# Performance work log

Hardware: AMD Instinct MI355X
Metric: run time of the kernel (lower is better)

The kernel has to match this reference:

```python
import jax, jax.numpy as jnp
import numpy as np

BETA = 0.01
EPS = 1e-6

def conv3x3(x, w, b):
    y = jax.lax.conv_general_dilated(x, w, (1, 1), 'SAME',
                                     dimension_numbers=('NCHW', 'OIHW', 'NCHW'))
    return y + b[None, :, None, None]

def variance_depth_flow(gt, patch, max_depth):
    B, C, H, W = gt.shape
    py, px = H // patch, W // patch
    # [B,C,py,px,P,P]
    p = gt.reshape(B, C, py, patch, px, patch).transpose(0, 1, 2, 4, 3, 5)
    p = jnp.where((p > 0.1) & (p < max_depth), p, jnp.zeros_like(p))
    bn = jnp.log(p[..., 0, :] + EPS)   # north border  [B,C,py,px,P]
    bs = jnp.log(p[..., -1, :] + EPS)  # south
    bw = jnp.log(p[..., :, 0] + EPS)   # west
    be = jnp.log(p[..., :, -1] + EPS)  # east
    def sx(b):  # shift patches left along x (axis=3), zero-pad last column
        return jnp.concatenate([b[:, :, :, 1:], jnp.zeros_like(b[:, :, :, :1])], axis=3)
    def sy(b):  # shift patches up along y (axis=2), zero-pad last row
        return jnp.concatenate([b[:, :, 1:], jnp.zeros_like(b[:, :, :1])], axis=2)
    diffs = [be - sx(bw), bs - sy(bn), be - sx(be), bs - sy(bs), bw - sx(bw),
             bn - sy(bn), bs - sx(bs), be - sy(be), bn - sx(bn), bw - sy(bw)]
    d = jnp.stack([x.sum(-1) for x in diffs], axis=-1)  # [B,C,py,px,10]
    d = d[:, 0].transpose(0, 3, 1, 2) / patch            # [B,10,py,px]
    return d

def smooth_l1(pred, target, beta):
    d = pred - target
    ad = jnp.abs(d)
    return jnp.where(ad < beta, 0.5 * d * d / beta, ad - 0.5 * beta)

def setup_inputs() -> dict:
    key = jax.random.key(0)
    ks = jax.random.split(key, 7)
    B, FC, DC, hw, HW = 32, 256, 64, 64, 512
    feat = jax.random.normal(ks[0], (B, FC, hw, hw), dtype=jnp.float32)
    depth = jax.random.normal(ks[1], (B, DC, hw, hw), dtype=jnp.float32)
    gts = jax.random.uniform(ks[2], (B, 1, HW, HW), dtype=jnp.float32)
    W_att = jax.random.normal(ks[3], (DC, FC, 3, 3), dtype=jnp.float32) * 0.02
    b_att = jnp.zeros((DC,), dtype=jnp.float32)
    W_post = jax.random.normal(ks[4], (10, DC, 3, 3), dtype=jnp.float32) * 0.05
    b_post = jnp.zeros((10,), dtype=jnp.float32)
    return {"feat": feat, "depth": depth, "gts": gts,
            "W_att": W_att, "b_att": b_att, "W_post": W_post, "b_post": b_post}

def reference(feat, depth, gts, W_att, b_att, W_post, b_post):
    max_depth = 80.0
    n, c, h, w = depth.shape
    patch = gts.shape[2] // h
    flow_gradient = variance_depth_flow(gts, patch, max_depth)  # [B,10,h,w]
    att = jax.nn.sigmoid(conv3x3(feat, W_att, b_att))           # [B,DC,h,w]
    ds = conv3x3(att * depth, W_post, b_post)                   # [B,10,h,w]
    diff = smooth_l1(ds, flow_gradient, BETA)
    return diff.sum() / (h * w * ds.shape[0] * ds.shape[1])
```

## Files before the change

kernel.cpp:

```cpp
#include <hip/hip_runtime.h>
#include <hip/hip_bf16.h>


typedef __attribute__((ext_vector_type(4))) float f32x4;
typedef __attribute__((ext_vector_type(8))) short s16x8;

#define DEVFN __device__ __forceinline__

DEVFN float bf2f(unsigned short u){
  unsigned int x = ((unsigned int)u) << 16;
  float f; __builtin_memcpy(&f, &x, 4); return f;
}
DEVFN unsigned short f2bf(float f){
  unsigned int x; __builtin_memcpy(&x, &f, 4);
  x += 0x7fffu + ((x >> 16) & 1u);
  return (unsigned short)(x >> 16);
}

#define ASYNC16(gp, lp) __builtin_amdgcn_global_load_lds( \
    (const __attribute__((address_space(1))) unsigned int*)(gp), \
    (__attribute__((address_space(3))) unsigned int*)(lp), 16, 0, 0)

__global__ void k_weights(const float* __restrict__ Watt, const float* __restrict__ Wpost,
                          unsigned short* __restrict__ WT1, unsigned short* __restrict__ WT2){
  const int t = blockIdx.x * 256 + threadIdx.x;
  const int n1 = 9 * 64 * 256;
  if (t < n1){
    const int tap = t / (64 * 256);
    const int rem = t % (64 * 256);
    const int oc = rem / 256, ic = rem % 256;
    WT1[t] = f2bf(Watt[(oc * 256 + ic) * 9 + tap]);
  }
  const int n2 = 9 * 16 * 64;
  if (t < n2){
    const int tap = t / (16 * 64);
    const int rem = t % (16 * 64);
    const int od = rem / 64, ic = rem % 64;
    const float v = (od < 10) ? Wpost[(od * 64 + ic) * 9 + tap] : 0.0f;
    WT2[t] = f2bf(v);
  }
}

__global__ void k_borders(const float* __restrict__ gts, float* __restrict__ S,
                          float* __restrict__ out){
  const int bid = blockIdx.x, tid = threadIdx.x;
  if (bid == 0 && tid == 0) *out = 0.0f;
  __shared__ float slab[4096];
  const int rel = bid;
  const float* gp = gts + (size_t)rel * 4096;
#pragma unroll
  for (int it = 0; it < 4; ++it){
    const int id = it * 256 + tid;
    *(f32x4*)&slab[id * 4] = *(const f32x4*)&gp[id * 4];
  }
  __syncthreads();
  const int px = tid & 63, border = tid >> 6;
  float s = 0.0f;
#pragma unroll
  for (int i = 0; i < 8; ++i){
    float v;
    if (border == 0)      v = slab[px * 8 + i];
    else if (border == 1) v = slab[7 * 512 + px * 8 + i];
    else if (border == 2) v = slab[i * 512 + px * 8];
    else                  v = slab[i * 512 + px * 8 + 7];
    v = ((v > 0.1f) && (v < 80.0f)) ? v : 0.0f;
    s += __logf(v + 1e-6f);
  }
  S[((size_t)rel * 64 + px) * 4 + border] = s;
}

__global__ __launch_bounds__(256, 2) void k_gemm1(
    const float* __restrict__ feat,
    const unsigned short* __restrict__ WT1,
    const float* __restrict__ batt,
    const float* __restrict__ depth,
    unsigned short* __restrict__ adT)
{
  __shared__ unsigned short As[6 * 66 * 32];
  __shared__ unsigned short Bs[576 * 32];
  const int t = threadIdx.x;
  const int l = t & 63, w = t >> 6;
  const int b = blockIdx.x >> 4, ytile = blockIdx.x & 15;
  const int y0 = ytile * 4;
  const int fr = l & 15, g = l >> 4;
  const int x = l;

  f32x4 acc[4][4];
#pragma unroll
  for (int i = 0; i < 4; ++i)
#pragma unroll
    for (int j = 0; j < 4; ++j)
#pragma unroll
      for (int q = 0; q < 4; ++q) acc[i][j][q] = 0.0f;

  if (t < 48){
    const int yy = t >> 3, k = t & 7;
    const int xp = (k & 1) ? 65 : 0;
    s16x8 z = {0,0,0,0,0,0,0,0};
    *(s16x8*)&As[(yy * 66 + xp) * 32 + (k >> 1) * 8] = z;
  }

  const int xp = x + 1;
  const int sx = (xp >> 1) & 3;
  const int slotB = (g ^ ((fr >> 1) & 3)) * 8;

  for (int c = 0; c < 8; ++c){
    float rr[48];
#pragma unroll
    for (int j = 0; j < 6; ++j){
      const int yr = y0 - 1 + j;
      if (yr >= 0 && yr < 64){
        const float* gp = feat + ((size_t)(b * 256 + c * 32 + w * 8)) * 4096
                               + (size_t)yr * 64 + x;
#pragma unroll
        for (int e = 0; e < 8; ++e) rr[j * 8 + e] = gp[(size_t)e * 4096];
      } else {
#pragma unroll
        for (int e = 0; e < 8; ++e) rr[j * 8 + e] = 0.0f;
      }
    }
#pragma unroll
    for (int it = 0; it < 9; ++it){
      const int idx = it * 256 + t;
      const int row = idx >> 2;
      const int sg = (idx & 3) ^ ((row >> 1) & 3);
      ASYNC16(WT1 + (size_t)row * 256 + c * 32 + sg * 8, &Bs[(size_t)idx * 8]);
    }
#pragma unroll
    for (int j = 0; j < 6; ++j){
      s16x8 v;
#pragma unroll
      for (int e = 0; e < 8; ++e) v[e] = (short)f2bf(rr[j * 8 + e]);
      *(s16x8*)&As[(j * 66 + xp) * 32 + ((w ^ sx) * 8)] = v;
    }
    __syncthreads();

    for (int tap = 0; tap < 9; ++tap){
      const int dy = tap / 3 - 1, dxp = tap % 3;
      const int r = fr + dxp;
      const int slotA = (g ^ ((r >> 1) & 3)) * 8;
      const int rowb = ((w + dy + 1) * 66 + r) * 32 + slotA;
      s16x8 af[4], bfr[4];
#pragma unroll
      for (int i = 0; i < 4; ++i) af[i] = *(const s16x8*)&As[rowb + i * 512];
#pragma unroll
      for (int j = 0; j < 4; ++j)
        bfr[j] = *(const s16x8*)&Bs[(tap * 64 + j * 16 + fr) * 32 + slotB];
#pragma unroll
      for (int i = 0; i < 4; ++i)
#pragma unroll
        for (int j = 0; j < 4; ++j)
          acc[i][j] = __builtin_amdgcn_mfma_f32_16x16x32_bf16(af[i], bfr[j], acc[i][j], 0, 0, 0);
    }
    __syncthreads();
  }

  const int y = y0 + w;
#pragma unroll
  for (int j = 0; j < 4; ++j){
    const int oc = j * 16 + fr;
    const float bb = batt[oc];
    const float* dpt = depth + ((size_t)(b * 64 + oc)) * 4096 + (size_t)y * 64;
    unsigned short* op = adT + ((size_t)(b * 4096 + y * 64)) * 64 + oc;
#pragma unroll
    for (int i = 0; i < 4; ++i){
#pragma unroll
      for (int q = 0; q < 4; ++q){
        const int xo = i * 16 + g * 4 + q;
        const float v = acc[i][j][q] + bb;
        const float att = 1.0f / (1.0f + __expf(-v));
        op[(size_t)xo * 64] = f2bf(att * dpt[xo]);
      }
    }
  }
}

DEVFN float sel4(f32x4 v, int i){
  const float ab = (i & 1) ? v[1] : v[0];
  const float cd = (i & 1) ? v[3] : v[2];
  return (i & 2) ? cd : ab;
}

__global__ __launch_bounds__(512, 2) void k_gemm2(
    const unsigned short* __restrict__ adT,
    const unsigned short* __restrict__ WT2,
    const float* __restrict__ bpost,
    const f32x4* __restrict__ S,
    float* __restrict__ out)
{
  __shared__ unsigned short As[2][20480];
  __shared__ unsigned short Bs[9216];
  __shared__ float ps[8];
  const int t = threadIdx.x;
  const int l = t & 63, w = t >> 6;
  const int b = blockIdx.x >> 3, ytile = blockIdx.x & 7;
  const int y0 = ytile * 8;
  const int fr = l & 15, g = l >> 4;

  f32x4 acc[4];
#pragma unroll
  for (int i = 0; i < 4; ++i)
#pragma unroll
    for (int q = 0; q < 4; ++q) acc[i][q] = 0.0f;

  auto stageA = [&](int c, int d){
#pragma unroll
    for (int it2 = 0; it2 < 5; ++it2){
      const int it = it2 * 2 + (t >> 8);
      const int yy = y0 - 1 + it;
      const int xx = (t >> 2) & 63, icg = t & 3;
      unsigned short* lp = &As[d][(it * 64 + xx) * 32 + icg * 8];
      if (yy >= 0 && yy < 64){
        const int sg = icg ^ ((xx >> 1) & 3);
        const unsigned short* gp = adT
            + ((size_t)(b * 4096 + yy * 64 + xx)) * 64 + c * 32 + sg * 8;
        ASYNC16(gp, lp);
      } else {
        s16x8 z = {0,0,0,0,0,0,0,0};
        *(s16x8*)lp = z;
      }
    }
  };
#pragma unroll
  for (int it = 0; it < 3; ++it){
    const int idx = it * 512 + t;
    if (idx < 1152){
      const int row = idx >> 3, p = idx & 7;
      const int sg = p ^ (row & 7);
      ASYNC16(WT2 + (size_t)row * 64 + sg * 8, Bs + (size_t)idx * 8);
    }
  }
  stageA(0, 0);
  __syncthreads();

  for (int c = 0; c < 2; ++c){
    if (c == 0) stageA(1, 1);
    const unsigned short* Ab = As[c];
    const int pB = ((c * 4 + g) ^ (fr & 7)) * 8;
    for (int tap = 0; tap < 9; ++tap){
      const int dy = tap / 3 - 1, dx = tap % 3 - 1;
      s16x8 af[4];
#pragma unroll
      for (int i = 0; i < 4; ++i){
        const int xv = i * 16 + fr + dx;
        const bool valid = (xv >= 0) && (xv < 64);
        const int xw = valid ? xv : 0;
        const int slot = (g ^ ((xw >> 1) & 3)) * 8;
        s16x8 v = *(const s16x8*)&Ab[((w + dy + 1) * 64 + xw) * 32 + slot];
        s16x8 z = {0,0,0,0,0,0,0,0};
        af[i] = valid ? v : z;
      }
      const s16x8 bfr = *(const s16x8*)&Bs[(tap * 16 + fr) * 64 + pB];
#pragma unroll
      for (int i = 0; i < 4; ++i)
        acc[i] = __builtin_amdgcn_mfma_f32_16x16x32_bf16(af[i], bfr, acc[i], 0, 0, 0);
    }
    __syncthreads();
  }

  const unsigned aPack = (3u<<0)|(1u<<2)|(3u<<4)|(1u<<6)|(2u<<8)|(0u<<10)|(1u<<12)|(3u<<14)|(0u<<16)|(2u<<18);
  const unsigned bPack = (2u<<0)|(0u<<2)|(3u<<4)|(1u<<6)|(2u<<8)|(0u<<10)|(1u<<12)|(3u<<14)|(0u<<16)|(2u<<18);
  float lsum = 0.0f;
  const int y = y0 + w;
  if (fr < 10){
    const int od = fr;
    const int ai = (aPack >> (2 * od)) & 3;
    const int bi = (bPack >> (2 * od)) & 3;
    const bool xshift = (od & 1) == 0;
    const float bp = bpost[od];
#pragma unroll
    for (int i = 0; i < 4; ++i){
#pragma unroll
      for (int q = 0; q < 4; ++q){
        const int xo = i * 16 + g * 4 + q;
        const size_t gm = (size_t)b * 4096 + (size_t)y * 64 + xo;
        const f32x4 sa = S[gm];
        const bool nb = xshift ? (xo < 63) : (y < 63);
        const size_t ga = xshift ? (nb ? gm + 1 : gm) : (nb ? gm + 64 : gm);
        const f32x4 sbv = S[ga];
        const float sbf = nb ? sel4(sbv, bi) : 0.0f;
        const float flow = (sel4(sa, ai) - sbf) * 0.125f;
        const float dv = acc[i][q] + bp - flow;
        const float adv = fabsf(dv);
        lsum += (adv < 0.01f) ? (50.0f * dv * dv) : (adv - 0.005f);
      }
    }
  }
#pragma unroll
  for (int off = 32; off > 0; off >>= 1) lsum += __shfl_down(lsum, off);
  if (l == 0) ps[w] = lsum;
  __syncthreads();
  if (t == 0){
    float s = 0.0f;
#pragma unroll
    for (int i = 0; i < 8; ++i) s += ps[i];
    atomicAdd(out, s * (1.0f / 1310720.0f));
  }
}

extern "C" void kernel_launch(void* const* d_in, const int* in_sizes, int n_in,
                              void* d_out, int out_size, void* d_ws, size_t ws_size,
                              hipStream_t stream){
  const float* feat  = (const float*)d_in[0];
  const float* depth = (const float*)d_in[1];
  const float* gts   = (const float*)d_in[2];
  const float* Watt  = (const float*)d_in[3];
  const float* batt  = (const float*)d_in[4];
  const float* Wpost = (const float*)d_in[5];
  const float* bpost = (const float*)d_in[6];
  float* out = (float*)d_out;
  char* ws = (char*)d_ws;

  unsigned short* adT = (unsigned short*)ws;
  unsigned short* WT1 = (unsigned short*)(ws + 16777216);
  unsigned short* WT2 = (unsigned short*)(ws + 16777216 + 294912);
  float*          S   = (float*)(ws + 16777216 + 294912 + 18432);

  k_weights<<<576, 256, 0, stream>>>(Watt, Wpost, WT1, WT2);
  k_gemm1<<<512, 256, 0, stream>>>(feat, WT1, batt, depth, adT);
  k_borders<<<2048, 256, 0, stream>>>(gts, S, out);
  k_gemm2<<<256, 512, 0, stream>>>(adT, WT2, bpost, (const f32x4*)S, out);
}
```

Before: 90.16 us.

## Pre-transpose features to bf16 NHWC and stream them into LDS asynchronously

Adds a separate kernel that converts the fp32 NCHW feature map into a bf16 channel-last, swizzled buffer. The conv GEMM can then fill its A tile with direct global-to-LDS async copies instead of strided per-channel fp32 loads and in-register conversion. The x-halo padding is replaced by masked fragment reads, and depth values are loaded as vectors in the epilogue. This costs an extra launch plus a full 64 MB write and read of the transposed features, in exchange for a lighter load path inside the GEMM.

```diff
diff --git a/kernel.cpp b/kernel.cpp
--- a/kernel.cpp
+++ b/kernel.cpp
@@ -15,6 +15,11 @@
   unsigned int x; __builtin_memcpy(&x, &f, 4);
   x += 0x7fffu + ((x >> 16) & 1u);
   return (unsigned short)(x >> 16);
+}
+DEVFN unsigned cvtpk(float lo, float hi){
+  unsigned r;
+  asm("v_cvt_pk_bf16_f32 %0, %1, %2" : "=v"(r) : "v"(lo), "v"(hi));
+  return r;
 }
 
 #define ASYNC16(gp, lp) __builtin_amdgcn_global_load_lds( \
@@ -41,6 +46,34 @@
   }
 }
 
+__global__ void k_transpose(const float* __restrict__ feat, unsigned short* __restrict__ featT){
+  __shared__ float lds[128][65];
+  const int bid = blockIdx.x;
+  const int cg = bid & 1;
+  const int y  = (bid >> 1) & 63;
+  const int b  = bid >> 7;
+  const int t = threadIdx.x;
+  const int x = t & 63, rg = t >> 6;
+  const float* sp = feat + ((size_t)(b * 256 + cg * 128)) * 4096 + (size_t)y * 64;
+#pragma unroll
+  for (int r = rg; r < 128; r += 4) lds[r][x] = sp[(size_t)r * 4096 + x];
+  __syncthreads();
+  const int ox = t >> 2, s = t & 3;
+  const int swz = (ox >> 1) & 3;
+  unsigned short* dp = featT + ((size_t)(b * 4096 + y * 64 + ox)) * 256 + cg * 128;
+#pragma unroll
+  for (int kk = 0; kk < 4; ++kk){
+    const int icb = kk * 32 + s * 8;
+    unsigned pk[4];
+#pragma unroll
+    for (int p = 0; p < 4; ++p)
+      pk[p] = cvtpk(lds[icb + 2 * p][ox], lds[icb + 2 * p + 1][ox]);
+    s16x8 v;
+    __builtin_memcpy(&v, pk, 16);
+    *(s16x8*)(dp + kk * 32 + ((s ^ swz) * 8)) = v;
+  }
+}
+
 __global__ void k_borders(const float* __restrict__ gts, float* __restrict__ S,
                           float* __restrict__ out){
   const int bid = blockIdx.x, tid = threadIdx.x;
@@ -70,20 +103,19 @@
 }
 
 __global__ __launch_bounds__(256, 2) void k_gemm1(
-    const float* __restrict__ feat,
+    const unsigned short* __restrict__ featT,
     const unsigned short* __restrict__ WT1,
     const float* __restrict__ batt,
     const float* __restrict__ depth,
     unsigned short* __restrict__ adT)
 {
-  __shared__ unsigned short As[6 * 66 * 32];
+  __shared__ unsigned short As[6 * 64 * 32];
   __shared__ unsigned short Bs[576 * 32];
   const int t = threadIdx.x;
   const int l = t & 63, w = t >> 6;
   const int b = blockIdx.x >> 4, ytile = blockIdx.x & 15;
   const int y0 = ytile * 4;
   const int fr = l & 15, g = l >> 4;
-  const int x = l;
 
   f32x4 acc[4][4];
 #pragma unroll
@@ -93,30 +125,20 @@
 #pragma unroll
       for (int q = 0; q < 4; ++q) acc[i][j][q] = 0.0f;
 
-  if (t < 48){
-    const int yy = t >> 3, k = t & 7;
-    const int xp = (k & 1) ? 65 : 0;
-    s16x8 z = {0,0,0,0,0,0,0,0};
-    *(s16x8*)&As[(yy * 66 + xp) * 32 + (k >> 1) * 8] = z;
-  }
-
-  const int xp = x + 1;
-  const int sx = (xp >> 1) & 3;
   const int slotB = (g ^ ((fr >> 1) & 3)) * 8;
 
   for (int c = 0; c < 8; ++c){
-    float rr[48];
-#pragma unroll
-    for (int j = 0; j < 6; ++j){
-      const int yr = y0 - 1 + j;
+#pragma unroll
+    for (int yy = 0; yy < 6; ++yy){
+      const int yr = y0 - 1 + yy;
+      unsigned short* lp = &As[yy * 2048 + t * 8];
       if (yr >= 0 && yr < 64){
-        const float* gp = feat + ((size_t)(b * 256 + c * 32 + w * 8)) * 4096
-                               + (size_t)yr * 64 + x;
-#pragma unroll
-        for (int e = 0; e < 8; ++e) rr[j * 8 + e] = gp[(size_t)e * 4096];
+        const unsigned short* gp = featT
+            + ((size_t)(b * 4096 + yr * 64 + (t >> 2))) * 256 + c * 32 + (t & 3) * 8;
+        ASYNC16(gp, lp);
       } else {
-#pragma unroll
-        for (int e = 0; e < 8; ++e) rr[j * 8 + e] = 0.0f;
+        s16x8 z = {0,0,0,0,0,0,0,0};
+        *(s16x8*)lp = z;
       }
     }
 #pragma unroll
@@ -126,23 +148,23 @@
       const int sg = (idx & 3) ^ ((row >> 1) & 3);
       ASYNC16(WT1 + (size_t)row * 256 + c * 32 + sg * 8, &Bs[(size_t)idx * 8]);
     }
-#pragma unroll
-    for (int j = 0; j < 6; ++j){
-      s16x8 v;
-#pragma unroll
-      for (int e = 0; e < 8; ++e) v[e] = (short)f2bf(rr[j * 8 + e]);
-      *(s16x8*)&As[(j * 66 + xp) * 32 + ((w ^ sx) * 8)] = v;
-    }
     __syncthreads();
 
+#pragma unroll
     for (int tap = 0; tap < 9; ++tap){
-      const int dy = tap / 3 - 1, dxp = tap % 3;
-      const int r = fr + dxp;
-      const int slotA = (g ^ ((r >> 1) & 3)) * 8;
-      const int rowb = ((w + dy + 1) * 66 + r) * 32 + slotA;
+      const int dy = tap / 3 - 1, dx = tap % 3 - 1;
+      const int yy = w + dy + 1;
       s16x8 af[4], bfr[4];
 #pragma unroll
-      for (int i = 0; i < 4; ++i) af[i] = *(const s16x8*)&As[rowb + i * 512];
+      for (int i = 0; i < 4; ++i){
+        const int xv = i * 16 + fr + dx;
+        const bool valid = (xv >= 0) && (xv < 64);
+        const int xw = valid ? xv : 0;
+        const int slot = (g ^ ((xw >> 1) & 3)) * 8;
+        s16x8 v = *(const s16x8*)&As[(yy * 64 + xw) * 32 + slot];
+        s16x8 z = {0,0,0,0,0,0,0,0};
+        af[i] = valid ? v : z;
+      }
 #pragma unroll
       for (int j = 0; j < 4; ++j)
         bfr[j] = *(const s16x8*)&Bs[(tap * 64 + j * 16 + fr) * 32 + slotB];
@@ -164,12 +186,13 @@
     unsigned short* op = adT + ((size_t)(b * 4096 + y * 64)) * 64 + oc;
 #pragma unroll
     for (int i = 0; i < 4; ++i){
+      const f32x4 dv4 = *(const f32x4*)&dpt[i * 16 + g * 4];
 #pragma unroll
       for (int q = 0; q < 4; ++q){
         const int xo = i * 16 + g * 4 + q;
         const float v = acc[i][j][q] + bb;
         const float att = 1.0f / (1.0f + __expf(-v));
-        op[(size_t)xo * 64] = f2bf(att * dpt[xo]);
+        op[(size_t)xo * 64] = f2bf(att * dv4[q]);
       }
     }
   }
@@ -311,13 +334,15 @@
   float* out = (float*)d_out;
   char* ws = (char*)d_ws;
 
-  unsigned short* adT = (unsigned short*)ws;
-  unsigned short* WT1 = (unsigned short*)(ws + 16777216);
-  unsigned short* WT2 = (unsigned short*)(ws + 16777216 + 294912);
-  float*          S   = (float*)(ws + 16777216 + 294912 + 18432);
+  unsigned short* featT = (unsigned short*)ws;
+  unsigned short* adT   = (unsigned short*)(ws + 67108864);
+  unsigned short* WT1   = (unsigned short*)(ws + 67108864 + 16777216);
+  unsigned short* WT2   = (unsigned short*)(ws + 67108864 + 16777216 + 294912);
+  float*          S     = (float*)(ws + 67108864 + 16777216 + 294912 + 18432);
 
   k_weights<<<576, 256, 0, stream>>>(Watt, Wpost, WT1, WT2);
-  k_gemm1<<<512, 256, 0, stream>>>(feat, WT1, batt, depth, adT);
+  k_transpose<<<4096, 256, 0, stream>>>(feat, featT);
+  k_gemm1<<<512, 256, 0, stream>>>(featT, WT1, batt, depth, adT);
   k_borders<<<2048, 256, 0, stream>>>(gts, S, out);
   k_gemm2<<<256, 512, 0, stream>>>(adT, WT2, bpost, (const f32x4*)S, out);
 }
```

Result: slower. 121.9 us (+35.2%).
